# Kernel tuning notes

Hardware: AMD Instinct MI355X
Metric: run time of the kernel (lower is better)

Reference implementation:

```python
import jax, jax.numpy as jnp
import numpy as np

ALPHA = 300.0  # attractor strength (exp variant: exp(-alpha*|dx|^gamma)*dx, gamma=2)


def setup_inputs() -> dict:
    key = jax.random.key(0)
    k0, k1, k2, k3 = jax.random.split(key, 4)
    n, c, h, w = 4, 256, 128, 128
    mlp_dim, n_attractors, n_bins = 128, 16, 64
    x = jax.random.normal(k0, (n, c, h, w), jnp.float32)
    b_prev = jax.random.uniform(k1, (n, n_bins, h, w), jnp.float32)  # bin centers
    w1 = jax.random.normal(k2, (mlp_dim, c), jnp.float32) * 0.02
    b1 = jnp.zeros((mlp_dim,), jnp.float32)
    w2 = jax.random.normal(k3, (n_attractors, mlp_dim), jnp.float32) * 0.02
    b2 = jnp.zeros((n_attractors,), jnp.float32)
    return {"x": x, "b_prev": b_prev, "w1": w1, "b1": b1, "w2": w2, "b2": b2}


def reference(x, b_prev, w1, b1, w2, b2):
    # 1x1 conv MLP head: Conv2d(c->mlp) -> ReLU -> Conv2d(mlp->n_attractors) -> Softplus
    hfeat = jax.nn.relu(jnp.einsum('nchw,oc->nohw', x, w1) + b1[None, :, None, None])
    A = jax.nn.softplus(jnp.einsum('nchw,oc->nohw', hfeat, w2) + b2[None, :, None, None])
    # b_prev interpolated to (h, w) == identity here (same spatial size)
    b_centers = b_prev
    # dx: [n, n_attractors, n_bins, h, w]
    dx = A[:, :, None, :, :] - b_centers[:, None, :, :, :]
    # exp attractor with gamma=2: exp(-alpha*dx^2) * dx, summed over attractors ('sum' kind)
    delta_c = jnp.sum(jnp.exp(-ALPHA * dx * dx) * dx, axis=1)
    b_new_centers = b_centers + delta_c
    return (b_new_centers, b_new_centers)
```

## Files before the change

kernel.cpp:

```cpp
#include <hip/hip_runtime.h>
#include <hip/hip_bf16.h>
#include <stdint.h>


#define HW 16384
#define ALPHA 300.0f
#define EXP2K -432.8085122666891f

typedef short bf16x8_t __attribute__((ext_vector_type(8)));
typedef float f32x4_t __attribute__((ext_vector_type(4)));
typedef float f32x2_t __attribute__((ext_vector_type(2)));
typedef unsigned int u32x4_t __attribute__((ext_vector_type(4)));

__device__ __forceinline__ unsigned short f2bf(float f) {
  unsigned int u = __builtin_bit_cast(unsigned int, f);
  u += 0x7fffu + ((u >> 16) & 1u);
  return (unsigned short)(u >> 16);
}
__device__ __forceinline__ unsigned int cvtpk(float lo, float hi) {
  unsigned int r;
  asm("v_cvt_pk_bf16_f32 %0, %1, %2" : "=v"(r) : "v"(lo), "v"(hi));
  return r;
}
__device__ __forceinline__ float exp2a(float x) {
  float r;
  asm("v_exp_f32 %0, %1" : "=v"(r) : "v"(x));
  return r;
}
__device__ __forceinline__ float aldo(unsigned int voff, const void* sbase) {
  float r;
  asm volatile("global_load_dword %0, %1, %2" : "=v"(r) : "v"(voff), "s"(sbase));
  return r;
}
__device__ __forceinline__ u32x4_t ald4o(unsigned int voff, const void* sbase) {
  u32x4_t r;
  asm volatile("global_load_dwordx4 %0, %1, %2" : "=v"(r) : "v"(voff), "s"(sbase));
  return r;
}

__global__ void zoed_prep(const float* __restrict__ w1,
                          const float* __restrict__ w2,
                          unsigned short* __restrict__ blob) {
  int i = blockIdx.x * 256 + threadIdx.x;
  if (i < 32768) {
    int o = i >> 8, c = i & 255;
    float v = w1[i];
    int idx = (c >> 5) * 4096 + o * 32 + ((((c >> 3) & 3) ^ (o & 3)) << 3) + (c & 7);
    blob[idx] = f2bf(v);
  } else {
    int i2 = i - 32768;
    int a = i2 >> 7, o = i2 & 127;
    float v = w2[i2];
    int idx = 32768 + (o >> 5) * 512 + a * 32 + ((((o >> 3) & 3) ^ (a & 3)) << 3) + (o & 7);
    blob[idx] = f2bf(v);
  }
}

#define KITER(KB, NWAIT, AFNEXT, XNEXT)                                     \
  {                                                                         \
    constexpr int kb = KB;                                                  \
    asm volatile("s_waitcnt vmcnt(" #NWAIT ")");                            \
    __builtin_amdgcn_sched_barrier(0);                                      \
    u32x4_t v = {cvtpk(xr[kb & 3][0], xr[kb & 3][1]),                       \
                 cvtpk(xr[kb & 3][2], xr[kb & 3][3]),                       \
                 cvtpk(xr[kb & 3][4], xr[kb & 3][5]),                       \
                 cvtpk(xr[kb & 3][6], xr[kb & 3][7])};                      \
    bf16x8_t bfm = __builtin_bit_cast(bf16x8_t, v);                         \
    _Pragma("unroll") for (int tm = 0; tm < 8; tm++)                        \
        acc[tm] = __builtin_amdgcn_mfma_f32_16x16x32_bf16(                  \
            __builtin_bit_cast(bf16x8_t, af[tm]), bfm, acc[tm], 0, 0, 0);   \
    __builtin_amdgcn_sched_barrier(0);                                      \
    if (AFNEXT) {                                                           \
      _Pragma("unroll") for (int tm = 0; tm < 8; tm++)                      \
          af[tm] =                                                          \
              ald4o(voffw + (unsigned)((kb + 1) * 8192 + tm * 1024), wblob);\
    }                                                                       \
    if (XNEXT) {                                                            \
      _Pragma("unroll") for (int j = 0; j < 8; j++)                         \
          xr[(kb + 3) & 3][j] =                                             \
              aldo(voffx + (unsigned)(((kb + 3) * 32 + j) * HW) * 4u, xs);  \
    }                                                                       \
  }

__global__ __launch_bounds__(256, 4) void zoed_fused(
    const float* __restrict__ x, const float* __restrict__ bprev,
    const float* __restrict__ b1, const float* __restrict__ b2,
    const unsigned short* __restrict__ wblob, float* __restrict__ out) {
  __shared__ __align__(16) char smem[21504];

  const int t = threadIdx.x;
  const int lane = t & 63;
  const int l15 = lane & 15;
  const int quad = lane >> 4;
  const int wv = t >> 6;
  const int sw = ((quad ^ (l15 & 3)) << 4);

  const int blk = blockIdx.x;
  const int n = blk >> 8;
  const int p0 = ((blk & 255) << 6) + wv * 16;

  char* hid = smem + wv * 4096;
  char* Ab = smem + 16384 + wv * 1280;

  const float* xs = x + (size_t)(n * 256) * HW;
  const unsigned voffx = (unsigned)((quad * 8) * HW + p0 + l15) * 4u;
  const unsigned voffw = (unsigned)(l15 * 64 + sw);

  u32x4_t af[8];
#pragma unroll
  for (int tm = 0; tm < 8; tm++) af[tm] = ald4o(voffw + tm * 1024, wblob);
  float xr[4][8];
#pragma unroll
  for (int c = 0; c < 3; c++)
#pragma unroll
    for (int j = 0; j < 8; j++)
      xr[c][j] = aldo(voffx + (unsigned)((c * 32 + j) * HW) * 4u, xs);

  f32x4_t acc[8];
#pragma unroll
  for (int i = 0; i < 8; i++) acc[i] = (f32x4_t){0.f, 0.f, 0.f, 0.f};

  KITER(0, 16, 1, 1)
  KITER(1, 8, 1, 1)
  KITER(2, 8, 1, 1)
  KITER(3, 8, 1, 1)
  KITER(4, 8, 1, 1)
  KITER(5, 8, 1, 0)
  KITER(6, 0, 1, 0)
  KITER(7, 0, 0, 0)

  size_t obase = (size_t)(n * 64 + quad * 16) * HW + p0 + l15;
  const float* bp = bprev + obase;
  float bpr[16];
#pragma unroll
  for (int b = 0; b < 16; b++) bpr[b] = bp[(size_t)b * HW];
  bf16x8_t a2[4];
#pragma unroll
  for (int kc = 0; kc < 4; kc++)
    a2[kc] = *(const bf16x8_t*)((const char*)wblob + 65536 + kc * 1024 +
                                l15 * 64 + sw);

#pragma unroll
  for (int tm = 0; tm < 8; tm++) {
    f32x4_t b1v = *(const f32x4_t*)(b1 + tm * 16 + quad * 4);
    f32x4_t h = acc[tm] + b1v;
    h[0] = fmaxf(h[0], 0.f);
    h[1] = fmaxf(h[1], 0.f);
    h[2] = fmaxf(h[2], 0.f);
    h[3] = fmaxf(h[3], 0.f);
    int kc = tm >> 1;
    int g = (tm & 1) * 2 + (quad >> 1);
    int off8 = (quad & 1) * 8;
    unsigned int* dst = (unsigned int*)(hid + kc * 1024 + l15 * 64 +
                                        ((g ^ (l15 & 3)) << 4) + off8);
    dst[0] = cvtpk(h[0], h[1]);
    dst[1] = cvtpk(h[2], h[3]);
  }
  f32x4_t acc2 = (f32x4_t){0.f, 0.f, 0.f, 0.f};
#pragma unroll
  for (int kc = 0; kc < 4; kc++) {
    bf16x8_t bh = *(const bf16x8_t*)(hid + kc * 1024 + l15 * 64 + sw);
    acc2 = __builtin_amdgcn_mfma_f32_16x16x32_bf16(a2[kc], bh, acc2, 0, 0, 0);
  }
  {
    f32x4_t b2v = *(const f32x4_t*)(b2 + quad * 4);
    f32x4_t z = acc2 + b2v;
    f32x4_t spv;
#pragma unroll
    for (int r = 0; r < 4; r++) {
      float zz = z[r];
      spv[r] = fmaxf(zz, 0.f) + log1pf(__expf(-fabsf(zz)));
    }
    *(f32x4_t*)(Ab + l15 * 80 + quad * 16) = spv;
  }
  f32x2_t av2[8];
#pragma unroll
  for (int q = 0; q < 4; q++) {
    f32x4_t v = *(const f32x4_t*)(Ab + l15 * 80 + q * 16);
    av2[q * 2] = (f32x2_t){v[0], v[1]};
    av2[q * 2 + 1] = (f32x2_t){v[2], v[3]};
  }
  const f32x2_t K2 = {EXP2K, EXP2K};
  float* o1 = out + obase;
  float* o2 = o1 + (size_t)256 * HW;
#pragma unroll
  for (int b = 0; b < 16; b++) {
    float c = bpr[b];
    f32x2_t c2 = {c, c};
    f32x2_t d0 = {0.f, 0.f}, d1 = {0.f, 0.f};
#pragma unroll
    for (int k = 0; k < 4; k++) {
      f32x2_t dx = av2[k] - c2;
      f32x2_t tt = dx * K2;
      f32x2_t arg = tt * dx;
      f32x2_t e = {exp2a(arg[0]), exp2a(arg[1])};
      d0 = e * dx + d0;
    }
#pragma unroll
    for (int k = 4; k < 8; k++) {
      f32x2_t dx = av2[k] - c2;
      f32x2_t tt = dx * K2;
      f32x2_t arg = tt * dx;
      f32x2_t e = {exp2a(arg[0]), exp2a(arg[1])};
      d1 = e * dx + d1;
    }
    f32x2_t ds = d0 + d1;
    float r = c + (ds[0] + ds[1]);
    __builtin_nontemporal_store(r, o1 + (size_t)b * HW);
    __builtin_nontemporal_store(r, o2 + (size_t)b * HW);
  }
}

extern "C" void kernel_launch(void* const* d_in, const int* in_sizes, int n_in,
                              void* d_out, int out_size, void* d_ws,
                              size_t ws_size, hipStream_t stream) {
  const float* x = (const float*)d_in[0];
  const float* bprev = (const float*)d_in[1];
  const float* w1 = (const float*)d_in[2];
  const float* b1 = (const float*)d_in[3];
  const float* w2 = (const float*)d_in[4];
  const float* b2 = (const float*)d_in[5];
  float* outp = (float*)d_out;
  unsigned short* blob = (unsigned short*)d_ws;

  zoed_prep<<<136, 256, 0, stream>>>(w1, w2, blob);
  zoed_fused<<<1024, 256, 0, stream>>>(x, bprev, b1, b2, blob, outp);
}
```

Baseline: 141.2 us.

## Split hidden-layer MLP work across wave pairs with 512-thread blocks

Each 16-pixel group is now handled by two waves instead of one. Each wave computes half of the 128 hidden channels and half of the 64 output bins, which halves per-wave accumulator and register use so more waves can be resident. The hand-scheduled inline-asm prefetch pipeline with explicit vmcnt waits is replaced by plain compiler-scheduled loads. The trade-off is that both waves of a pair load the same x slice, doubling cache traffic for x, and two block-wide barriers are added around the second layer, which only half the waves compute.

```diff
diff --git a/kernel.cpp b/kernel.cpp
--- a/kernel.cpp
+++ b/kernel.cpp
@@ -27,16 +27,6 @@
   asm("v_exp_f32 %0, %1" : "=v"(r) : "v"(x));
   return r;
 }
-__device__ __forceinline__ float aldo(unsigned int voff, const void* sbase) {
-  float r;
-  asm volatile("global_load_dword %0, %1, %2" : "=v"(r) : "v"(voff), "s"(sbase));
-  return r;
-}
-__device__ __forceinline__ u32x4_t ald4o(unsigned int voff, const void* sbase) {
-  u32x4_t r;
-  asm volatile("global_load_dwordx4 %0, %1, %2" : "=v"(r) : "v"(voff), "s"(sbase));
-  return r;
-}
 
 __global__ void zoed_prep(const float* __restrict__ w1,
                           const float* __restrict__ w2,
@@ -56,33 +46,7 @@
   }
 }
 
-#define KITER(KB, NWAIT, AFNEXT, XNEXT)                                     \
-  {                                                                         \
-    constexpr int kb = KB;                                                  \
-    asm volatile("s_waitcnt vmcnt(" #NWAIT ")");                            \
-    __builtin_amdgcn_sched_barrier(0);                                      \
-    u32x4_t v = {cvtpk(xr[kb & 3][0], xr[kb & 3][1]),                       \
-                 cvtpk(xr[kb & 3][2], xr[kb & 3][3]),                       \
-                 cvtpk(xr[kb & 3][4], xr[kb & 3][5]),                       \
-                 cvtpk(xr[kb & 3][6], xr[kb & 3][7])};                      \
-    bf16x8_t bfm = __builtin_bit_cast(bf16x8_t, v);                         \
-    _Pragma("unroll") for (int tm = 0; tm < 8; tm++)                        \
-        acc[tm] = __builtin_amdgcn_mfma_f32_16x16x32_bf16(                  \
-            __builtin_bit_cast(bf16x8_t, af[tm]), bfm, acc[tm], 0, 0, 0);   \
-    __builtin_amdgcn_sched_barrier(0);                                      \
-    if (AFNEXT) {                                                           \
-      _Pragma("unroll") for (int tm = 0; tm < 8; tm++)                      \
-          af[tm] =                                                          \
-              ald4o(voffw + (unsigned)((kb + 1) * 8192 + tm * 1024), wblob);\
-    }                                                                       \
-    if (XNEXT) {                                                            \
-      _Pragma("unroll") for (int j = 0; j < 8; j++)                         \
-          xr[(kb + 3) & 3][j] =                                             \
-              aldo(voffx + (unsigned)(((kb + 3) * 32 + j) * HW) * 4u, xs);  \
-    }                                                                       \
-  }
-
-__global__ __launch_bounds__(256, 4) void zoed_fused(
+__global__ __launch_bounds__(512, 8) void zoed_fused(
     const float* __restrict__ x, const float* __restrict__ bprev,
     const float* __restrict__ b1, const float* __restrict__ b2,
     const unsigned short* __restrict__ wblob, float* __restrict__ out) {
@@ -93,62 +57,50 @@
   const int l15 = lane & 15;
   const int quad = lane >> 4;
   const int wv = t >> 6;
+  const int pg = wv >> 1;
+  const int half = wv & 1;
   const int sw = ((quad ^ (l15 & 3)) << 4);
 
   const int blk = blockIdx.x;
   const int n = blk >> 8;
-  const int p0 = ((blk & 255) << 6) + wv * 16;
+  const int p0 = ((blk & 255) << 6) + pg * 16;
 
-  char* hid = smem + wv * 4096;
-  char* Ab = smem + 16384 + wv * 1280;
+  char* hid = smem + pg * 5376;
+  char* Ab = smem + pg * 5376 + 4096;
 
-  const float* xs = x + (size_t)(n * 256) * HW;
-  const unsigned voffx = (unsigned)((quad * 8) * HW + p0 + l15) * 4u;
-  const unsigned voffw = (unsigned)(l15 * 64 + sw);
+  const float* xb = x + (size_t)(n * 256 + quad * 8) * HW + p0 + l15;
+  const char* wb = (const char*)wblob + half * 4096 + l15 * 64 + sw;
 
-  u32x4_t af[8];
+  f32x4_t acc[4];
 #pragma unroll
-  for (int tm = 0; tm < 8; tm++) af[tm] = ald4o(voffw + tm * 1024, wblob);
-  float xr[4][8];
-#pragma unroll
-  for (int c = 0; c < 3; c++)
-#pragma unroll
-    for (int j = 0; j < 8; j++)
-      xr[c][j] = aldo(voffx + (unsigned)((c * 32 + j) * HW) * 4u, xs);
-
-  f32x4_t acc[8];
-#pragma unroll
-  for (int i = 0; i < 8; i++) acc[i] = (f32x4_t){0.f, 0.f, 0.f, 0.f};
-
-  KITER(0, 16, 1, 1)
-  KITER(1, 8, 1, 1)
-  KITER(2, 8, 1, 1)
-  KITER(3, 8, 1, 1)
-  KITER(4, 8, 1, 1)
-  KITER(5, 8, 1, 0)
-  KITER(6, 0, 1, 0)
-  KITER(7, 0, 0, 0)
-
-  size_t obase = (size_t)(n * 64 + quad * 16) * HW + p0 + l15;
-  const float* bp = bprev + obase;
-  float bpr[16];
-#pragma unroll
-  for (int b = 0; b < 16; b++) bpr[b] = bp[(size_t)b * HW];
-  bf16x8_t a2[4];
-#pragma unroll
-  for (int kc = 0; kc < 4; kc++)
-    a2[kc] = *(const bf16x8_t*)((const char*)wblob + 65536 + kc * 1024 +
-                                l15 * 64 + sw);
+  for (int i = 0; i < 4; i++) acc[i] = (f32x4_t){0.f, 0.f, 0.f, 0.f};
 
 #pragma unroll
-  for (int tm = 0; tm < 8; tm++) {
-    f32x4_t b1v = *(const f32x4_t*)(b1 + tm * 16 + quad * 4);
+  for (int kb = 0; kb < 8; ++kb) {
+    float xv[8];
+#pragma unroll
+    for (int j = 0; j < 8; j++) xv[j] = xb[(size_t)(kb * 32 + j) * HW];
+    u32x4_t v = {cvtpk(xv[0], xv[1]), cvtpk(xv[2], xv[3]),
+                 cvtpk(xv[4], xv[5]), cvtpk(xv[6], xv[7])};
+    bf16x8_t bfm = __builtin_bit_cast(bf16x8_t, v);
+#pragma unroll
+    for (int tm = 0; tm < 4; tm++) {
+      bf16x8_t af = *(const bf16x8_t*)(wb + kb * 8192 + tm * 1024);
+      acc[tm] = __builtin_amdgcn_mfma_f32_16x16x32_bf16(af, bfm, acc[tm],
+                                                        0, 0, 0);
+    }
+  }
+
+#pragma unroll
+  for (int tm = 0; tm < 4; tm++) {
+    f32x4_t b1v = *(const f32x4_t*)(b1 + half * 64 + tm * 16 + quad * 4);
     f32x4_t h = acc[tm] + b1v;
     h[0] = fmaxf(h[0], 0.f);
     h[1] = fmaxf(h[1], 0.f);
     h[2] = fmaxf(h[2], 0.f);
     h[3] = fmaxf(h[3], 0.f);
-    int kc = tm >> 1;
+    int tg = half * 4 + tm;
+    int kc = tg >> 1;
     int g = (tm & 1) * 2 + (quad >> 1);
     int off8 = (quad & 1) * 8;
     unsigned int* dst = (unsigned int*)(hid + kc * 1024 + l15 * 64 +
@@ -156,13 +108,24 @@
     dst[0] = cvtpk(h[0], h[1]);
     dst[1] = cvtpk(h[2], h[3]);
   }
-  f32x4_t acc2 = (f32x4_t){0.f, 0.f, 0.f, 0.f};
+
+  size_t obase = (size_t)(n * 64 + half * 32 + quad * 8) * HW + p0 + l15;
+  const float* bp = bprev + obase;
+  float bpr[8];
 #pragma unroll
-  for (int kc = 0; kc < 4; kc++) {
-    bf16x8_t bh = *(const bf16x8_t*)(hid + kc * 1024 + l15 * 64 + sw);
-    acc2 = __builtin_amdgcn_mfma_f32_16x16x32_bf16(a2[kc], bh, acc2, 0, 0, 0);
-  }
-  {
+  for (int b = 0; b < 8; b++) bpr[b] = bp[(size_t)b * HW];
+
+  __syncthreads();
+
+  if (half == 0) {
+    f32x4_t acc2 = (f32x4_t){0.f, 0.f, 0.f, 0.f};
+#pragma unroll
+    for (int kc = 0; kc < 4; kc++) {
+      bf16x8_t a2 = *(const bf16x8_t*)((const char*)wblob + 65536 +
+                                       kc * 1024 + l15 * 64 + sw);
+      bf16x8_t bh = *(const bf16x8_t*)(hid + kc * 1024 + l15 * 64 + sw);
+      acc2 = __builtin_amdgcn_mfma_f32_16x16x32_bf16(a2, bh, acc2, 0, 0, 0);
+    }
     f32x4_t b2v = *(const f32x4_t*)(b2 + quad * 4);
     f32x4_t z = acc2 + b2v;
     f32x4_t spv;
@@ -173,6 +136,8 @@
     }
     *(f32x4_t*)(Ab + l15 * 80 + quad * 16) = spv;
   }
+  __syncthreads();
+
   f32x2_t av2[8];
 #pragma unroll
   for (int q = 0; q < 4; q++) {
@@ -184,7 +149,7 @@
   float* o1 = out + obase;
   float* o2 = o1 + (size_t)256 * HW;
 #pragma unroll
-  for (int b = 0; b < 16; b++) {
+  for (int b = 0; b < 8; b++) {
     float c = bpr[b];
     f32x2_t c2 = {c, c};
     f32x2_t d0 = {0.f, 0.f}, d1 = {0.f, 0.f};
@@ -224,5 +189,5 @@
   unsigned short* blob = (unsigned short*)d_ws;
 
   zoed_prep<<<136, 256, 0, stream>>>(w1, w2, blob);
-  zoed_fused<<<1024, 256, 0, stream>>>(x, bprev, b1, b2, blob, outp);
+  zoed_fused<<<1024, 512, 0, stream>>>(x, bprev, b1, b2, blob, outp);
 }
```

New measurement: 152.5 us. 8.0% more time.
